# Kernel optimization log

Hardware: AMD Instinct MI355X
Metric: run time of the kernel (lower is better)

## Reference

```python
import jax, jax.numpy as jnp
import numpy as np

N_NODES = 100000
N_EDGES = 1000000

def _gcn_conv(x, W, b, src, dst, n_nodes):
    # PyG GCNConv: linear first, then symmetric-normalized aggregation with self loops
    x = x @ W  # [N, F_out]
    loop = jnp.arange(n_nodes, dtype=src.dtype)
    src2 = jnp.concatenate([src, loop])
    dst2 = jnp.concatenate([dst, loop])
    deg = jax.ops.segment_sum(jnp.ones(src2.shape[0], x.dtype), dst2, num_segments=n_nodes)
    dinv = jnp.where(deg > 0, jax.lax.rsqrt(deg), 0.0)
    norm = dinv[src2] * dinv[dst2]  # [E+N]
    msgs = x[src2] * norm[:, None]  # gather + scale
    out = jax.ops.segment_sum(msgs, dst2, num_segments=n_nodes)  # scatter-add
    return out + b

def _pair_norm_si(x):
    # mode 'PN-SI', scale=1
    x = x - x.mean(axis=0)
    row_norm = jnp.sqrt(1e-6 + jnp.sum(x * x, axis=1, keepdims=True))
    return x / row_norm

def setup_inputs() -> dict:
    key = jax.random.key(0)
    k1, k2, k3, k4 = jax.random.split(key, 4)
    in_c, hid_c, out_c = 256, 64, 40
    x = jax.random.normal(k1, (N_NODES, in_c), dtype=jnp.float32)
    edge_index = jax.random.randint(k2, (2, N_EDGES), 0, N_NODES, dtype=jnp.int64)
    W1 = jax.random.normal(k3, (in_c, hid_c), dtype=jnp.float32) / np.sqrt(in_c)
    b1 = jnp.zeros((hid_c,), jnp.float32)
    W2 = jax.random.normal(k4, (hid_c, out_c), dtype=jnp.float32) / np.sqrt(hid_c)
    b2 = jnp.zeros((out_c,), jnp.float32)
    return {"x": x, "edge_index": edge_index, "W1": W1, "b1": b1, "W2": W2, "b2": b2}

def reference(x, edge_index, W1, b1, W2, b2):
    src, dst = edge_index[0], edge_index[1]
    n = x.shape[0]
    h = jax.nn.relu(_gcn_conv(x, W1, b1, src, dst, n))
    h = _gcn_conv(h, W2, b2, src, dst, n)
    h = _pair_norm_si(h)
    return jax.nn.log_softmax(h, axis=1)
```

## Files before the change

### kernel.cpp

```cpp
#include <hip/hip_runtime.h>
#include <hip/hip_fp16.h>
#include <math.h>

#define F_IN  256
#define F_HID 64
#define F_OUT 40
#define HS2_LD 64

typedef _Float16 h8 __attribute__((ext_vector_type(8)));
typedef float f4 __attribute__((ext_vector_type(4)));

__global__ void k_degw(const int* __restrict__ dst, unsigned* __restrict__ degc, int E,
                       const float* __restrict__ W1, const float* __restrict__ W2,
                       __half* __restrict__ Wt, __half* __restrict__ W2t) {
    int i = blockIdx.x * 256 + threadIdx.x;
    if (i < E) {
        int d = __builtin_nontemporal_load(dst + i);
        atomicAdd(&degc[d], 1u);
        return;
    }
    int j = i - E;
    if (j < 16384) {
        int k = j >> 6, n = j & 63;
        Wt[n * 256 + k] = __float2half(W1[j]);
    } else if (j < 20480) {
        int jj = j - 16384;
        int n = jj >> 6, k = jj & 63;
        W2t[n * 64 + k] = __float2half((n < F_OUT) ? W2[k * F_OUT + n] : 0.f);
    }
}

__global__ __launch_bounds__(256) void k_scan(const unsigned* __restrict__ degc,
                                              unsigned* __restrict__ aggf,
                                              unsigned* __restrict__ ticket,
                                              unsigned* __restrict__ rowptr,
                                              float* __restrict__ dinv,
                                              unsigned* __restrict__ cursor,
                                              float* __restrict__ colsum, int N) {
    __shared__ unsigned s[256];
    __shared__ unsigned sTick, sPfx, sTot;
    int tid = threadIdx.x;
    if (tid == 0) sTick = atomicAdd(ticket, 1u);
    if (blockIdx.x == 0 && tid < 64) colsum[tid] = 0.f;
    __syncthreads();
    unsigned b = sTick;
    int i = (int)b * 256 + tid;
    unsigned d = (i < N) ? degc[i] : 0u;
    unsigned v = (i < N) ? ((d + 8u) & ~7u) : 0u;
    s[tid] = v;
    __syncthreads();
    for (int off = 1; off < 256; off <<= 1) {
        unsigned t = (tid >= off) ? s[tid - off] : 0u;
        __syncthreads();
        s[tid] += t;
        __syncthreads();
    }
    unsigned incl = s[tid];
    if (tid == 255) {
        sTot = s[255];
        atomicExch(&aggf[b], s[255] | 0x40000000u);
    }
    __syncthreads();
    if (tid < 64) {
        int lane = tid;
        unsigned run = 0;
        int base = (int)b - 1;
        while (base >= 0) {
            int idx = base - lane;
            unsigned t = 0;
            if (idx >= 0) {
                do { t = atomicAdd(&aggf[idx], 0u); } while ((t >> 30) == 0u);
            }
            unsigned long long pmask = __ballot(idx >= 0 && (t >> 30) == 3u);
            if (pmask) {
                int L = __ffsll((unsigned long long)pmask) - 1;
                unsigned contrib = (lane <= L) ? (t & 0x3FFFFFFFu) : 0u;
                #pragma unroll
                for (int off = 32; off >= 1; off >>= 1) contrib += __shfl_xor(contrib, off, 64);
                run += contrib;
                break;
            } else {
                unsigned contrib = (idx >= 0) ? (t & 0x3FFFFFFFu) : 0u;
                #pragma unroll
                for (int off = 32; off >= 1; off >>= 1) contrib += __shfl_xor(contrib, off, 64);
                run += contrib;
                base -= 64;
            }
        }
        if (lane == 0) {
            sPfx = run;
            atomicExch(&aggf[b], (run + sTot) | 0xC0000000u);
        }
    }
    __syncthreads();
    unsigned pfx = sPfx;
    if (i < N) {
        rowptr[i] = pfx + incl - v;
        dinv[i] = rsqrtf((float)d + 1.0f);
        cursor[i] = 0u;
        if (i == N - 1) rowptr[N] = pfx + incl;
    }
    if (i == 0) dinv[N] = 1.0f;
}

#define FILLB 1024
__global__ __launch_bounds__(256) void k_fillmm1(const int* __restrict__ src, const int* __restrict__ dst,
                          const unsigned* __restrict__ degc,
                          const unsigned* __restrict__ rowptr, unsigned* __restrict__ cursor,
                          unsigned* __restrict__ colp,
                          const float* __restrict__ x, const __half* __restrict__ Wth,
                          const float* __restrict__ dinv, __half* __restrict__ hs1o,
                          int E, int N) {
    int tid = threadIdx.x;
    if ((int)blockIdx.x < FILLB) {
        int r  = blockIdx.x & 3;
        int sb = blockIdx.x >> 2;
        int S  = FILLB >> 2;
        int lo = (int)(((long long)N * r) >> 2);
        int hi = (int)(((long long)N * (r + 1)) >> 2);
        int stride = S * 256;
        for (int t = sb * 256 + tid; t < E; t += stride) {
            int d = __builtin_nontemporal_load(dst + t);
            if (d >= lo && d < hi) {
                int sv = __builtin_nontemporal_load(src + t);
                unsigned p = atomicAdd(&cursor[d], 1u);
                colp[rowptr[d] + p] = (unsigned)sv;
            }
        }
        int npad = (hi - lo) * 8;
        for (int z = sb * 256 + tid; z < npad; z += stride) {
            int i = lo + (z >> 3), j = z & 7;
            unsigned d = degc[i];
            unsigned slot = d + (unsigned)j;
            if (slot < ((d + 8u) & ~7u))
                colp[rowptr[i] + slot] = (j == 0) ? (unsigned)i : (unsigned)N;
        }
        return;
    }
    const _Float16* Wt = (const _Float16*)Wth;
    _Float16* hs1 = (_Float16*)hs1o;
    int lane = tid & 63;
    int wv = tid >> 6;
    int m15 = lane & 15;
    int q = lane >> 4;
    int node0 = ((int)blockIdx.x - FILLB) * 64 + wv * 16;
    int arow = node0 + m15;
    bool ok = (arow < N);
    const f4* xr = (const f4*)(x + (size_t)arow * F_IN + q * 8);

    f4 acc[4];
    #pragma unroll
    for (int nt = 0; nt < 4; ++nt) acc[nt] = (f4){0.f, 0.f, 0.f, 0.f};

    #pragma unroll
    for (int kt = 0; kt < 8; ++kt) {
        f4 v0, v1;
        if (ok) {
            v0 = __builtin_nontemporal_load(xr + kt * 8);
            v1 = __builtin_nontemporal_load(xr + kt * 8 + 1);
        } else {
            v0 = (f4){0.f, 0.f, 0.f, 0.f};
            v1 = v0;
        }
        h8 a = { (_Float16)v0[0], (_Float16)v0[1], (_Float16)v0[2], (_Float16)v0[3],
                 (_Float16)v1[0], (_Float16)v1[1], (_Float16)v1[2], (_Float16)v1[3] };
        #pragma unroll
        for (int nt = 0; nt < 4; ++nt) {
            h8 b = *(const h8*)(Wt + (nt * 16 + m15) * 256 + kt * 32 + q * 8);
            acc[nt] = __builtin_amdgcn_mfma_f32_16x16x32_f16(a, b, acc[nt], 0, 0, 0);
        }
    }

    #pragma unroll
    for (int nt = 0; nt < 4; ++nt) {
        #pragma unroll
        for (int rr = 0; rr < 4; ++rr) {
            int node = node0 + q * 4 + rr;
            if (node <= N) {
                float din = (node < N) ? dinv[node] : 1.0f;
                hs1[(size_t)node * F_HID + nt * 16 + m15] = (_Float16)(acc[nt][rr] * din);
            }
        }
    }
}

#define AS 72
__global__ __launch_bounds__(256) void k_agg1mm2(const unsigned* __restrict__ rowptr,
                                                 const unsigned* __restrict__ colp,
                                                 const float* __restrict__ dinv,
                                                 const __half* __restrict__ hs1o,
                                                 const float* __restrict__ bias1,
                                                 const __half* __restrict__ W2th,
                                                 __half* __restrict__ hs2o, int N) {
    __shared__ _Float16 sA[64 * AS];
    const _Float16* hp = (const _Float16*)hs1o;
    const _Float16* W2t = (const _Float16*)W2th;
    _Float16* hs2 = (_Float16*)hs2o;
    int tid = threadIdx.x;
    int lane = tid & 63;
    int wv = tid >> 6;
    int g = lane >> 3, c = lane & 7;
    int nbase = blockIdx.x * 64;

    float bv[8];
    *(float4*)&bv[0] = *(const float4*)(bias1 + c * 8);
    *(float4*)&bv[4] = *(const float4*)(bias1 + c * 8 + 4);

    for (int it = 0; it < 4; ++it) {
        int n0 = nbase + wv * 16 + it * 4;

        float acc[4][8];
        #pragma unroll
        for (int s = 0; s < 4; ++s)
            #pragma unroll
            for (int j = 0; j < 8; ++j) acc[s][j] = 0.f;

        unsigned e[4], en[4], idx[4];
        #pragma unroll
        for (int s = 0; s < 4; ++s) {
            int nd = n0 + s;
            if (nd < N) { e[s] = rowptr[nd]; en[s] = rowptr[nd + 1]; }
            else        { e[s] = 0; en[s] = 0; }
        }
        #pragma unroll
        for (int s = 0; s < 4; ++s) {
            unsigned ec = (e[s] < en[s]) ? e[s] : (en[s] - 8u);
            ec = (ec > e[s]) ? e[s] : ec;
            idx[s] = colp[ec + g];
        }

        while (e[0] < en[0] || e[1] < en[1] || e[2] < en[2] || e[3] < en[3]) {
            float msk[4];
            h8 v[4];
            #pragma unroll
            for (int s = 0; s < 4; ++s) msk[s] = (e[s] < en[s]) ? 1.f : 0.f;
            #pragma unroll
            for (int s = 0; s < 4; ++s) v[s] = *(const h8*)(hp + (size_t)idx[s] * F_HID + c * 8);
            #pragma unroll
            for (int s = 0; s < 4; ++s) {
                e[s] += 8;
                unsigned ec = (e[s] < en[s]) ? e[s] : (en[s] - 8u);
                ec = (ec > e[s]) ? e[s] : ec;
                idx[s] = colp[ec + g];
            }
            #pragma unroll
            for (int s = 0; s < 4; ++s)
                #pragma unroll
                for (int j = 0; j < 8; ++j) acc[s][j] += (float)v[s][j] * msk[s];
        }

        #pragma unroll
        for (int off = 8; off <= 32; off <<= 1)
            #pragma unroll
            for (int s = 0; s < 4; ++s)
                #pragma unroll
                for (int j = 0; j < 8; ++j) acc[s][j] += __shfl_xor(acc[s][j], off, 64);

        if (g == 0) {
            #pragma unroll
            for (int s = 0; s < 4; ++s) {
                int nd = n0 + s;
                int row = wv * 16 + it * 4 + s;
                h8 ho;
                if (nd < N) {
                    float din = dinv[nd];
                    #pragma unroll
                    for (int j = 0; j < 8; ++j) ho[j] = (_Float16)fmaxf(acc[s][j] * din + bv[j], 0.f);
                } else {
                    ho = (h8){0, 0, 0, 0, 0, 0, 0, 0};
                }
                *(h8*)&sA[row * AS + c * 8] = ho;
            }
        }
    }
    __syncthreads();

    int m15 = lane & 15;
    int q = lane >> 4;
    h8 bf[2];
    #pragma unroll
    for (int kt = 0; kt < 2; ++kt)
        bf[kt] = *(const h8*)(W2t + (wv * 16 + m15) * 64 + kt * 32 + q * 8);

    f4 acc2[4];
    #pragma unroll
    for (int mt = 0; mt < 4; ++mt) acc2[mt] = (f4){0.f, 0.f, 0.f, 0.f};
    #pragma unroll
    for (int kt = 0; kt < 2; ++kt) {
        #pragma unroll
        for (int mt = 0; mt < 4; ++mt) {
            h8 a = *(const h8*)&sA[(mt * 16 + m15) * AS + kt * 32 + q * 8];
            acc2[mt] = __builtin_amdgcn_mfma_f32_16x16x32_f16(a, bf[kt], acc2[mt], 0, 0, 0);
        }
    }

    #pragma unroll
    for (int mt = 0; mt < 4; ++mt) {
        #pragma unroll
        for (int r = 0; r < 4; ++r) {
            int node = nbase + mt * 16 + q * 4 + r;
            if (node <= N) {
                float din = (node < N) ? dinv[node] : 1.0f;
                hs2[(size_t)node * HS2_LD + wv * 16 + m15] = (_Float16)(acc2[mt][r] * din);
            }
        }
    }
}

__global__ __launch_bounds__(256) void k_agg2(const unsigned* __restrict__ rowptr,
                                              const unsigned* __restrict__ colp,
                                              const float* __restrict__ dinv,
                                              const __half* __restrict__ hs2o,
                                              float* __restrict__ out,
                                              float* __restrict__ colsum, int N) {
    __shared__ float part[4][8][8];
    const _Float16* hp = (const _Float16*)hs2o;
    int lane = threadIdx.x & 63;
    int wv = threadIdx.x >> 6;
    int g = lane >> 3, c = lane & 7;
    int nwaves = gridDim.x * 4;
    float csum[8];
    #pragma unroll
    for (int j = 0; j < 8; ++j) csum[j] = 0.f;

    for (int w = blockIdx.x * 4 + wv; 4 * w < N; w += nwaves) {
        int n0 = 4 * w;
        float acc[4][8];
        #pragma unroll
        for (int s = 0; s < 4; ++s)
            #pragma unroll
            for (int j = 0; j < 8; ++j) acc[s][j] = 0.f;

        unsigned e[4], en[4], idx[4];
        #pragma unroll
        for (int s = 0; s < 4; ++s) {
            int nd = n0 + s;
            if (nd < N) { e[s] = rowptr[nd]; en[s] = rowptr[nd + 1]; }
            else        { e[s] = 0; en[s] = 0; }
        }
        #pragma unroll
        for (int s = 0; s < 4; ++s) {
            unsigned ec = (e[s] < en[s]) ? e[s] : (en[s] - 8u);
            ec = (ec > e[s]) ? e[s] : ec;
            idx[s] = colp[ec + g];
        }

        while (e[0] < en[0] || e[1] < en[1] || e[2] < en[2] || e[3] < en[3]) {
            float msk[4];
            h8 v[4];
            #pragma unroll
            for (int s = 0; s < 4; ++s) msk[s] = (e[s] < en[s]) ? 1.f : 0.f;
            #pragma unroll
            for (int s = 0; s < 4; ++s) v[s] = *(const h8*)(hp + (size_t)idx[s] * HS2_LD + c * 8);
            #pragma unroll
            for (int s = 0; s < 4; ++s) {
                e[s] += 8;
                unsigned ec = (e[s] < en[s]) ? e[s] : (en[s] - 8u);
                ec = (ec > e[s]) ? e[s] : ec;
                idx[s] = colp[ec + g];
            }
            #pragma unroll
            for (int s = 0; s < 4; ++s)
                #pragma unroll
                for (int j = 0; j < 8; ++j) acc[s][j] += (float)v[s][j] * msk[s];
        }

        #pragma unroll
        for (int off = 8; off <= 32; off <<= 1)
            #pragma unroll
            for (int s = 0; s < 4; ++s)
                #pragma unroll
                for (int j = 0; j < 8; ++j) acc[s][j] += __shfl_xor(acc[s][j], off, 64);

        if (g == 0) {
            #pragma unroll
            for (int s = 0; s < 4; ++s) {
                int nd = n0 + s;
                if (nd < N) {
                    float din = dinv[nd];
                    #pragma unroll
                    for (int j = 0; j < 8; ++j) { acc[s][j] *= din; csum[j] += acc[s][j]; }
                    if (c < 5) {
                        *(float4*)(out + (size_t)nd * F_OUT + c * 8) =
                            make_float4(acc[s][0], acc[s][1], acc[s][2], acc[s][3]);
                        *(float4*)(out + (size_t)nd * F_OUT + c * 8 + 4) =
                            make_float4(acc[s][4], acc[s][5], acc[s][6], acc[s][7]);
                    }
                }
            }
        }
    }

    if (g == 0) {
        #pragma unroll
        for (int j = 0; j < 8; ++j) part[wv][c][j] = csum[j];
    }
    __syncthreads();
    int tid = threadIdx.x;
    if (tid < F_OUT) {
        int cc = tid >> 3, jj = tid & 7;
        float s = part[0][cc][jj] + part[1][cc][jj] + part[2][cc][jj] + part[3][cc][jj];
        atomicAdd(&colsum[tid], s);
    }
}

__global__ __launch_bounds__(128) void k_final(float* __restrict__ out,
                                               const float* __restrict__ colsum, int N) {
    __shared__ float sMean[F_OUT];
    if (threadIdx.x < F_OUT) sMean[threadIdx.x] = colsum[threadIdx.x] * (1.0f / (float)N);
    __syncthreads();
    int n = blockIdx.x * blockDim.x + threadIdx.x;
    if (n >= N) return;
    float* row = out + (size_t)n * F_OUT;
    float4 vr[10];
    float ss = 0.f;
    #pragma unroll
    for (int b = 0; b < 10; ++b) {
        float4 t = *(const float4*)(row + b * 4);
        t.x -= sMean[b * 4 + 0]; t.y -= sMean[b * 4 + 1];
        t.z -= sMean[b * 4 + 2]; t.w -= sMean[b * 4 + 3];
        vr[b] = t;
        ss += t.x * t.x + t.y * t.y + t.z * t.z + t.w * t.w;
    }
    float scale = 1.0f / sqrtf(ss + 1e-6f);
    float m = -1e30f;
    #pragma unroll
    for (int b = 0; b < 10; ++b) {
        vr[b].x *= scale; vr[b].y *= scale; vr[b].z *= scale; vr[b].w *= scale;
        m = fmaxf(m, fmaxf(fmaxf(vr[b].x, vr[b].y), fmaxf(vr[b].z, vr[b].w)));
    }
    float sum = 0.f;
    #pragma unroll
    for (int b = 0; b < 10; ++b)
        sum += expf(vr[b].x - m) + expf(vr[b].y - m) + expf(vr[b].z - m) + expf(vr[b].w - m);
    float mlse = m + logf(sum);
    #pragma unroll
    for (int b = 0; b < 10; ++b) {
        float4 t = vr[b];
        t.x -= mlse; t.y -= mlse; t.z -= mlse; t.w -= mlse;
        *(float4*)(row + b * 4) = t;
    }
}

extern "C" void kernel_launch(void* const* d_in, const int* in_sizes, int n_in,
                              void* d_out, int out_size, void* d_ws, size_t ws_size,
                              hipStream_t stream) {
    const float* x  = (const float*)d_in[0];
    const int*   ei = (const int*)d_in[1];
    const float* W1 = (const float*)d_in[2];
    const float* b1 = (const float*)d_in[3];
    const float* W2 = (const float*)d_in[4];
    float* out = (float*)d_out;

    int N = in_sizes[0] / F_IN;
    int E = in_sizes[1] / 2;
    const int* src = ei;
    const int* dst = ei + E;

    char* p = (char*)d_ws;
    auto alloc = [&](size_t bytes) { char* r = p; p += (bytes + 127) & ~(size_t)127; return r; };
    unsigned* degc   = (unsigned*)alloc((size_t)N * 4);
    unsigned* aggf   = (unsigned*)alloc(512 * 4);
    unsigned* ticket = (unsigned*)alloc(4);
    char* zend = p;
    unsigned* cursor = (unsigned*)alloc((size_t)N * 4);
    float*    colsum = (float*)   alloc(64 * 4);
    unsigned* rowptr = (unsigned*)alloc((size_t)(N + 1) * 4);
    unsigned* colp   = (unsigned*)alloc((size_t)(E + 8 * N + 8) * 4);
    float*    dinv   = (float*)   alloc((size_t)(N + 1) * 4);
    __half*   hs1    = (__half*)  alloc((size_t)64 * (N + 1) * 2);
    __half*   hs2    = (__half*)  alloc((size_t)64 * (N + 1) * 2);
    __half*   Wt     = (__half*)  alloc((size_t)16384 * 2);
    __half*   W2t    = (__half*)  alloc((size_t)4096 * 2);

    hipMemsetAsync(d_ws, 0, (size_t)(zend - (char*)d_ws), stream);

    int nA = (N + 255) / 256;
    k_degw<<<(E + 20480 + 255) / 256, 256, 0, stream>>>(dst, degc, E, W1, W2, Wt, W2t);
    k_scan<<<nA, 256, 0, stream>>>(degc, aggf, ticket, rowptr, dinv, cursor, colsum, N);
    int MB = (N + 63) / 64;
    k_fillmm1<<<FILLB + MB, 256, 0, stream>>>(src, dst, degc, rowptr, cursor, colp,
                                              x, Wt, dinv, hs1, E, N);
    k_agg1mm2<<<(N + 64) / 64, 256, 0, stream>>>(rowptr, colp, dinv, hs1, b1, W2t, hs2, N);
    k_agg2<<<2048, 256, 0, stream>>>(rowptr, colp, dinv, hs2, out, colsum, N);
    k_final<<<(N + 127) / 128, 128, 0, stream>>>(out, colsum, N);
}
```

Before: 400.0 us.

## Split fused CSR fill and first matmul into separate kernels

Splits the combined CSR-fill/GEMM kernel back into two launches: a fill kernel with 2048 blocks and 8 destination ranges, and a standalone MFMA matmul kernel. It also drops the nontemporal load hints on the dst/src and x reads. The aim is to rebalance work and cut the atomic contention per range, at the cost of one more launch and losing overlap between the memory-bound matmul and the atomic-bound fill. With 8 ranges each fill block reads every dst entry, so the dst read traffic doubles.

```diff
diff --git a/kernel.cpp b/kernel.cpp
--- a/kernel.cpp
+++ b/kernel.cpp
@@ -15,8 +15,7 @@
                        __half* __restrict__ Wt, __half* __restrict__ W2t) {
     int i = blockIdx.x * 256 + threadIdx.x;
     if (i < E) {
-        int d = __builtin_nontemporal_load(dst + i);
-        atomicAdd(&degc[d], 1u);
+        atomicAdd(&degc[dst[i]], 1u);
         return;
     }
     int j = i - E;
@@ -103,50 +102,49 @@
     if (i == 0) dinv[N] = 1.0f;
 }
 
-#define FILLB 1024
-__global__ __launch_bounds__(256) void k_fillmm1(const int* __restrict__ src, const int* __restrict__ dst,
+__global__ __launch_bounds__(256) void k_fillpad(const int* __restrict__ src, const int* __restrict__ dst,
                           const unsigned* __restrict__ degc,
                           const unsigned* __restrict__ rowptr, unsigned* __restrict__ cursor,
-                          unsigned* __restrict__ colp,
-                          const float* __restrict__ x, const __half* __restrict__ Wth,
-                          const float* __restrict__ dinv, __half* __restrict__ hs1o,
-                          int E, int N) {
+                          unsigned* __restrict__ colp, int E, int N) {
+    int r  = blockIdx.x & 7;
+    int sb = blockIdx.x >> 3;
+    int S  = gridDim.x >> 3;
+    int lo = (int)(((long long)N * r) >> 3);
+    int hi = (int)(((long long)N * (r + 1)) >> 3);
     int tid = threadIdx.x;
-    if ((int)blockIdx.x < FILLB) {
-        int r  = blockIdx.x & 3;
-        int sb = blockIdx.x >> 2;
-        int S  = FILLB >> 2;
-        int lo = (int)(((long long)N * r) >> 2);
-        int hi = (int)(((long long)N * (r + 1)) >> 2);
-        int stride = S * 256;
-        for (int t = sb * 256 + tid; t < E; t += stride) {
-            int d = __builtin_nontemporal_load(dst + t);
-            if (d >= lo && d < hi) {
-                int sv = __builtin_nontemporal_load(src + t);
-                unsigned p = atomicAdd(&cursor[d], 1u);
-                colp[rowptr[d] + p] = (unsigned)sv;
-            }
-        }
-        int npad = (hi - lo) * 8;
-        for (int z = sb * 256 + tid; z < npad; z += stride) {
-            int i = lo + (z >> 3), j = z & 7;
-            unsigned d = degc[i];
-            unsigned slot = d + (unsigned)j;
-            if (slot < ((d + 8u) & ~7u))
-                colp[rowptr[i] + slot] = (j == 0) ? (unsigned)i : (unsigned)N;
-        }
-        return;
-    }
+    int stride = S * 256;
+    for (int t = sb * 256 + tid; t < E; t += stride) {
+        int d = dst[t];
+        if (d >= lo && d < hi) {
+            unsigned p = atomicAdd(&cursor[d], 1u);
+            colp[rowptr[d] + p] = (unsigned)src[t];
+        }
+    }
+    int npad = (hi - lo) * 8;
+    for (int z = sb * 256 + tid; z < npad; z += stride) {
+        int i = lo + (z >> 3), j = z & 7;
+        unsigned d = degc[i];
+        unsigned slot = d + (unsigned)j;
+        if (slot < ((d + 8u) & ~7u))
+            colp[rowptr[i] + slot] = (j == 0) ? (unsigned)i : (unsigned)N;
+    }
+}
+
+__global__ __launch_bounds__(256) void k_mm1(const float* __restrict__ x,
+                                             const __half* __restrict__ Wth,
+                                             const float* __restrict__ dinv,
+                                             __half* __restrict__ hs1o, int N) {
     const _Float16* Wt = (const _Float16*)Wth;
     _Float16* hs1 = (_Float16*)hs1o;
+    int tid = threadIdx.x;
     int lane = tid & 63;
     int wv = tid >> 6;
     int m15 = lane & 15;
     int q = lane >> 4;
-    int node0 = ((int)blockIdx.x - FILLB) * 64 + wv * 16;
+    int node0 = blockIdx.x * 64 + wv * 16;
     int arow = node0 + m15;
     bool ok = (arow < N);
-    const f4* xr = (const f4*)(x + (size_t)arow * F_IN + q * 8);
+    const float* xr = x + (size_t)arow * F_IN + q * 8;
 
     f4 acc[4];
     #pragma unroll
@@ -154,16 +152,16 @@
 
     #pragma unroll
     for (int kt = 0; kt < 8; ++kt) {
-        f4 v0, v1;
+        float4 v0, v1;
         if (ok) {
-            v0 = __builtin_nontemporal_load(xr + kt * 8);
-            v1 = __builtin_nontemporal_load(xr + kt * 8 + 1);
+            v0 = *(const float4*)(xr + kt * 32);
+            v1 = *(const float4*)(xr + kt * 32 + 4);
         } else {
-            v0 = (f4){0.f, 0.f, 0.f, 0.f};
+            v0 = make_float4(0.f, 0.f, 0.f, 0.f);
             v1 = v0;
         }
-        h8 a = { (_Float16)v0[0], (_Float16)v0[1], (_Float16)v0[2], (_Float16)v0[3],
-                 (_Float16)v1[0], (_Float16)v1[1], (_Float16)v1[2], (_Float16)v1[3] };
+        h8 a = { (_Float16)v0.x, (_Float16)v0.y, (_Float16)v0.z, (_Float16)v0.w,
+                 (_Float16)v1.x, (_Float16)v1.y, (_Float16)v1.z, (_Float16)v1.w };
         #pragma unroll
         for (int nt = 0; nt < 4; ++nt) {
             h8 b = *(const h8*)(Wt + (nt * 16 + m15) * 256 + kt * 32 + q * 8);
@@ -478,9 +476,8 @@
     int nA = (N + 255) / 256;
     k_degw<<<(E + 20480 + 255) / 256, 256, 0, stream>>>(dst, degc, E, W1, W2, Wt, W2t);
     k_scan<<<nA, 256, 0, stream>>>(degc, aggf, ticket, rowptr, dinv, cursor, colsum, N);
-    int MB = (N + 63) / 64;
-    k_fillmm1<<<FILLB + MB, 256, 0, stream>>>(src, dst, degc, rowptr, cursor, colp,
-                                              x, Wt, dinv, hs1, E, N);
+    k_fillpad<<<2048, 256, 0, stream>>>(src, dst, degc, rowptr, cursor, colp, E, N);
+    k_mm1<<<(N + 63) / 64, 256, 0, stream>>>(x, Wt, dinv, hs1, N);
     k_agg1mm2<<<(N + 64) / 64, 256, 0, stream>>>(rowptr, colp, dinv, hs1, b1, W2t, hs2, N);
     k_agg2<<<2048, 256, 0, stream>>>(rowptr, colp, dinv, hs2, out, colsum, N);
     k_final<<<(N + 127) / 128, 128, 0, stream>>>(out, colsum, N);
```

Result: no change. 398.6 us (-0.4%).
